# Performance work log

Hardware: AMD Instinct MI355X
Metric: run time of the kernel (lower is better)

The kernel has to match this reference:

```python
import jax, jax.numpy as jnp
import numpy as np

N = 50000      # nodes
E = 800000     # edges
IN = 128       # in_ch
OUT = 32       # out_ch
H = 4          # heads
ED = 16        # edge_dim
SLOPE = 0.2    # LeakyReLU negative slope (GATv2 default and outer activation)


def setup_inputs() -> dict:
    key = jax.random.key(0)
    ks = jax.random.split(key, 10)
    s_in = 1.0 / np.sqrt(IN)
    s_ed = 1.0 / np.sqrt(ED)
    s_out = 1.0 / np.sqrt(OUT)
    return {
        "x": jax.random.normal(ks[0], (N, IN), jnp.float32),
        "edge_index": jax.random.randint(ks[1], (2, E), 0, N, dtype=jnp.int32),
        "edges_attr": jax.random.normal(ks[2], (E, ED), jnp.float32),
        "W_l": jax.random.normal(ks[3], (IN, H * OUT), jnp.float32) * s_in,
        "b_l": jnp.zeros((H * OUT,), jnp.float32),
        "W_r": jax.random.normal(ks[4], (IN, H * OUT), jnp.float32) * s_in,
        "b_r": jnp.zeros((H * OUT,), jnp.float32),
        "W_e": jax.random.normal(ks[5], (ED, H * OUT), jnp.float32) * s_ed,
        "att": jax.random.normal(ks[6], (H, OUT), jnp.float32) * s_out,
        "bias": jnp.zeros((OUT,), jnp.float32),
    }


def reference(x, edge_index, edges_attr, W_l, b_l, W_r, b_r, W_e, att, bias):
    src, tgt = edge_index[0], edge_index[1]

    # add_self_loops with fill_value='mean': self-loop attr = scatter-mean of
    # incoming edge attrs per target node (0 for isolated nodes, as in PyG).
    deg = jax.ops.segment_sum(jnp.ones((E,), x.dtype), tgt, num_segments=N)
    attr_sum = jax.ops.segment_sum(edges_attr, tgt, num_segments=N)
    loop_attr = attr_sum / jnp.maximum(deg, 1.0)[:, None]
    node_ids = jnp.arange(N, dtype=src.dtype)
    src_f = jnp.concatenate([src, node_ids])   # [E+N]
    tgt_f = jnp.concatenate([tgt, node_ids])   # [E+N]
    attr_f = jnp.concatenate([edges_attr, loop_attr], axis=0)  # [E+N, ED]

    x_l = (x @ W_l + b_l).reshape(N, H, OUT)   # source transform
    x_r = (x @ W_r + b_r).reshape(N, H, OUT)   # target transform
    e = (attr_f @ W_e).reshape(-1, H, OUT)     # edge transform

    # GATv2 score: att . leaky_relu(x_l[j] + x_r[i] + e_ij)
    m = x_l[src_f] + x_r[tgt_f] + e                          # [E+N, H, OUT]
    scores = jnp.einsum('ehc,hc->eh', jax.nn.leaky_relu(m, SLOPE), att)

    # scatter-softmax over edges grouped by target node (every segment has a
    # self-loop, so segment_max is well-defined)
    smax = jax.ops.segment_max(scores, tgt_f, num_segments=N)
    ex = jnp.exp(scores - smax[tgt_f])
    denom = jax.ops.segment_sum(ex, tgt_f, num_segments=N)
    alpha = ex / denom[tgt_f]                                # [E+N, H]

    # weighted aggregation of source messages x_l[j]
    msg = alpha[:, :, None] * x_l[src_f]                     # [E+N, H, OUT]
    out = jax.ops.segment_sum(msg, tgt_f, num_segments=N)   # [N, H, OUT]

    out = out.mean(axis=1) + bias                            # concat=False -> head mean
    return jax.nn.leaky_relu(out, SLOPE)                     # outer LeakyReLU(0.2)
```

## Files before the change

kernel.cpp:

```cpp
#include <hip/hip_runtime.h>
#include <math.h>

#define NN 50000
#define NE 800000
#define SLOPE 0.2f
#define NB 49
#define GEMMB 782
#define EDGEB 3125


__device__ __forceinline__ void gemm_body(int bx, const float* __restrict__ x,
                                          const float* __restrict__ W,
                                          const float* __restrict__ bptr,
                                          float* __restrict__ optr,
                                          float* xs, float* wsm) {
  int tid = threadIdx.x;
  int cx = tid & 31;
  int rn = tid >> 5;
  int n0 = bx * 64;

  float acc[8][4];
#pragma unroll
  for (int i = 0; i < 8; ++i)
#pragma unroll
    for (int j = 0; j < 4; ++j) acc[i][j] = 0.f;

  for (int kb = 0; kb < 128; kb += 64) {
#pragma unroll
    for (int r = 0; r < 4; ++r) {
      int q = tid + r * 256;
      int n = q >> 4, k4 = q & 15;
      float4 v = make_float4(0.f, 0.f, 0.f, 0.f);
      int gn = n0 + n;
      if (gn < NN) v = *(const float4*)(x + (size_t)gn * 128 + kb + 4 * k4);
      *(float4*)&xs[n * 68 + 4 * k4] = v;
    }
#pragma unroll
    for (int r = 0; r < 8; ++r) {
      int q = tid + r * 256;
      int kk = q >> 5, c4 = q & 31;
      float4 wv = *(const float4*)(W + (size_t)(kb + kk) * 128 + 4 * c4);
      *(float4*)&wsm[kk * 128 + 4 * c4] = wv;
    }
    __syncthreads();
#pragma unroll 2
    for (int k4 = 0; k4 < 16; ++k4) {
      float4 wv[4];
#pragma unroll
      for (int kk = 0; kk < 4; ++kk)
        wv[kk] = *(const float4*)&wsm[(4 * k4 + kk) * 128 + 4 * cx];
#pragma unroll
      for (int i = 0; i < 8; ++i) {
        float4 xv = *(const float4*)&xs[(8 * rn + i) * 68 + 4 * k4];
        acc[i][0] = fmaf(xv.x, wv[0].x, acc[i][0]);
        acc[i][1] = fmaf(xv.x, wv[0].y, acc[i][1]);
        acc[i][2] = fmaf(xv.x, wv[0].z, acc[i][2]);
        acc[i][3] = fmaf(xv.x, wv[0].w, acc[i][3]);
        acc[i][0] = fmaf(xv.y, wv[1].x, acc[i][0]);
        acc[i][1] = fmaf(xv.y, wv[1].y, acc[i][1]);
        acc[i][2] = fmaf(xv.y, wv[1].z, acc[i][2]);
        acc[i][3] = fmaf(xv.y, wv[1].w, acc[i][3]);
        acc[i][0] = fmaf(xv.z, wv[2].x, acc[i][0]);
        acc[i][1] = fmaf(xv.z, wv[2].y, acc[i][1]);
        acc[i][2] = fmaf(xv.z, wv[2].z, acc[i][2]);
        acc[i][3] = fmaf(xv.z, wv[2].w, acc[i][3]);
        acc[i][0] = fmaf(xv.w, wv[3].x, acc[i][0]);
        acc[i][1] = fmaf(xv.w, wv[3].y, acc[i][1]);
        acc[i][2] = fmaf(xv.w, wv[3].z, acc[i][2]);
        acc[i][3] = fmaf(xv.w, wv[3].w, acc[i][3]);
      }
    }
    __syncthreads();
  }

  int cc = 4 * cx;
  float4 bv = *(const float4*)(bptr + cc);
#pragma unroll
  for (int i = 0; i < 8; ++i) {
    int gn = n0 + 8 * rn + i;
    if (gn < NN) {
      float4 o = make_float4(acc[i][0] + bv.x, acc[i][1] + bv.y,
                             acc[i][2] + bv.z, acc[i][3] + bv.w);
      *(float4*)(optr + (size_t)gn * 128 + cc) = o;
    }
  }
}


__launch_bounds__(256)
__global__ void fusedA_kernel(const float* __restrict__ x,
                              const float* __restrict__ W_l, const float* __restrict__ b_l,
                              float* __restrict__ x_l,
                              const int* __restrict__ tgt, int* __restrict__ deg,
                              int* __restrict__ rank) {
  __shared__ float xs[64 * 68];
  __shared__ float wsm[64 * 128];
  if (blockIdx.x < GEMMB) {
    gemm_body(blockIdx.x, x, W_l, b_l, x_l, xs, wsm);
  } else {
    int e = (blockIdx.x - GEMMB) * 256 + threadIdx.x;
    if (e < NE) rank[e] = atomicAdd(&deg[tgt[e]], 1);
  }
}


__launch_bounds__(256)
__global__ void fusedB_kernel(const float* __restrict__ x,
                              const float* __restrict__ W_r, const float* __restrict__ b_r,
                              float* __restrict__ x_r,
                              const int* __restrict__ src, const int* __restrict__ tgt,
                              const int* __restrict__ rank,
                              const int* __restrict__ rowptr,
                              const float4* __restrict__ eattr4,
                              int* __restrict__ csr_src,
                              float4* __restrict__ eattr_csr4) {
  __shared__ float xs[64 * 68];
  __shared__ float wsm[64 * 128];
  if (blockIdx.x < GEMMB) {
    gemm_body(blockIdx.x, x, W_r, b_r, x_r, xs, wsm);
  } else {
    int e = (blockIdx.x - GEMMB) * 256 + threadIdx.x;
    if (e < NE) {
      int t = tgt[e];
      int r = rank[e];
      float4 a0 = eattr4[(size_t)e * 4 + 0];
      float4 a1 = eattr4[(size_t)e * 4 + 1];
      float4 a2 = eattr4[(size_t)e * 4 + 2];
      float4 a3 = eattr4[(size_t)e * 4 + 3];
      int pos = rowptr[t] + r;
      csr_src[pos] = src[e];
      eattr_csr4[(size_t)pos * 4 + 0] = a0;
      eattr_csr4[(size_t)pos * 4 + 1] = a1;
      eattr_csr4[(size_t)pos * 4 + 2] = a2;
      eattr_csr4[(size_t)pos * 4 + 3] = a3;
    }
  }
}


__global__ void partial_kernel(const int* __restrict__ deg, int* __restrict__ psum) {
  int b = blockIdx.x;
  int base = b * 1024 + threadIdx.x * 4;
  int s = 0;
  if (base + 3 < NN) {
    int4 v = *(const int4*)(deg + base);
    s = v.x + v.y + v.z + v.w;
  } else {
#pragma unroll
    for (int i = 0; i < 4; ++i)
      if (base + i < NN) s += deg[base + i];
  }
  s += __shfl_xor(s, 1);
  s += __shfl_xor(s, 2);
  s += __shfl_xor(s, 4);
  s += __shfl_xor(s, 8);
  s += __shfl_xor(s, 16);
  s += __shfl_xor(s, 32);
  __shared__ int wsum[4];
  if ((threadIdx.x & 63) == 0) wsum[threadIdx.x >> 6] = s;
  __syncthreads();
  if (threadIdx.x == 0) psum[b] = wsum[0] + wsum[1] + wsum[2] + wsum[3];
}

__global__ void final_kernel(const int* __restrict__ deg, const int* __restrict__ psum,
                             int* __restrict__ rowptr) {
  __shared__ int offs_s;
  __shared__ int wtot[4];
  int b = blockIdx.x;
  int t = threadIdx.x;
  if (t < 64) {
    int lane = t;
    int mine = (lane < NB) ? psum[lane] : 0;
    int v = mine;
#pragma unroll
    for (int off = 1; off < 64; off <<= 1) {
      int u = __shfl_up(v, off);
      if (lane >= off) v += u;
    }
    if (lane == b) offs_s = v - mine;
    if (b == 0 && lane == 63) rowptr[NN] = v;
  }
  __syncthreads();

  int base = b * 1024 + t * 4;
  int d0 = 0, d1 = 0, d2 = 0, d3 = 0;
  if (base + 3 < NN) {
    int4 v = *(const int4*)(deg + base);
    d0 = v.x; d1 = v.y; d2 = v.z; d3 = v.w;
  } else {
    if (base < NN) d0 = deg[base];
    if (base + 1 < NN) d1 = deg[base + 1];
    if (base + 2 < NN) d2 = deg[base + 2];
  }
  int s = d0 + d1 + d2 + d3;
  int lane = t & 63, w = t >> 6;
  int v = s;
#pragma unroll
  for (int off = 1; off < 64; off <<= 1) {
    int u = __shfl_up(v, off);
    if (lane >= off) v += u;
  }
  if (lane == 63) wtot[w] = v;
  __syncthreads();
  int woff = 0;
#pragma unroll
  for (int i = 0; i < 4; ++i)
    if (i < w) woff += wtot[i];
  int run = offs_s + woff + (v - s);
  if (base < NN)     { rowptr[base] = run;     run += d0; }
  if (base + 1 < NN) { rowptr[base + 1] = run; run += d1; }
  if (base + 2 < NN) { rowptr[base + 2] = run; run += d2; }
  if (base + 3 < NN) { rowptr[base + 3] = run; }
}


#define EDGE_PROC(AV, XL)                                              \
  {                                                                    \
    float e0 = AV[0] * wek[0].x;                                       \
    e0 = fmaf(AV[1], wek[1].x, e0);   e0 = fmaf(AV[2], wek[2].x, e0);  \
    e0 = fmaf(AV[3], wek[3].x, e0);   e0 = fmaf(AV[4], wek[4].x, e0);  \
    e0 = fmaf(AV[5], wek[5].x, e0);   e0 = fmaf(AV[6], wek[6].x, e0);  \
    e0 = fmaf(AV[7], wek[7].x, e0);   e0 = fmaf(AV[8], wek[8].x, e0);  \
    e0 = fmaf(AV[9], wek[9].x, e0);   e0 = fmaf(AV[10], wek[10].x, e0);\
    e0 = fmaf(AV[11], wek[11].x, e0); e0 = fmaf(AV[12], wek[12].x, e0);\
    e0 = fmaf(AV[13], wek[13].x, e0); e0 = fmaf(AV[14], wek[14].x, e0);\
    e0 = fmaf(AV[15], wek[15].x, e0);                                  \
    float e1 = AV[0] * wek[0].y;                                       \
    e1 = fmaf(AV[1], wek[1].y, e1);   e1 = fmaf(AV[2], wek[2].y, e1);  \
    e1 = fmaf(AV[3], wek[3].y, e1);   e1 = fmaf(AV[4], wek[4].y, e1);  \
    e1 = fmaf(AV[5], wek[5].y, e1);   e1 = fmaf(AV[6], wek[6].y, e1);  \
    e1 = fmaf(AV[7], wek[7].y, e1);   e1 = fmaf(AV[8], wek[8].y, e1);  \
    e1 = fmaf(AV[9], wek[9].y, e1);   e1 = fmaf(AV[10], wek[10].y, e1);\
    e1 = fmaf(AV[11], wek[11].y, e1); e1 = fmaf(AV[12], wek[12].y, e1);\
    e1 = fmaf(AV[13], wek[13].y, e1); e1 = fmaf(AV[14], wek[14].y, e1);\
    e1 = fmaf(AV[15], wek[15].y, e1);                                  \
    es0 += e0; es1 += e1;                                              \
    float m0 = (XL.x + xr.x) + e0;                                     \
    float m1 = (XL.y + xr.y) + e1;                                     \
    float lm0 = fmaf(SLOPE, fminf(m0, 0.f), fmaxf(m0, 0.f));           \
    float lm1 = fmaf(SLOPE, fminf(m1, 0.f), fmaxf(m1, 0.f));           \
    float part = fmaf(attv.y, lm1, attv.x * lm0);                      \
    part += __shfl_xor(part, 1);                                       \
    part += __shfl_xor(part, 2);                                       \
    part += __shfl_xor(part, 4);                                       \
    part += __shfl_xor(part, 8);                                       \
    float p = __expf(part);                                            \
    lh += p;                                                           \
    acc0 = fmaf(p, XL.x, acc0);                                        \
    acc1 = fmaf(p, XL.y, acc1);                                        \
  }

__launch_bounds__(256)
__global__ void gat_kernel(const float* __restrict__ x_l, const float* __restrict__ x_r,
                           const int* __restrict__ rowptr, const int* __restrict__ csr_src,
                           const float* __restrict__ eattr_csr, const float* __restrict__ W_e,
                           const float* __restrict__ att, const float* __restrict__ bias,
                           float* __restrict__ out) {
  int wid = threadIdx.x >> 6;
  int lane = threadIdx.x & 63;
  int tbase = (blockIdx.x * 4 + wid) * 4;

  float2 wek[16];
#pragma unroll
  for (int k = 0; k < 16; ++k)
    wek[k] = *(const float2*)(W_e + k * 128 + 2 * lane);
  float2 attv = *(const float2*)(att + 2 * lane);
  float bv = bias[(2 * lane) & 31];
  float bv1 = bias[((2 * lane) & 31) + 1];

  for (int tt = 0; tt < 4; ++tt) {
    int t = tbase + tt;
    float2 xr = *(const float2*)(x_r + (size_t)t * 128 + 2 * lane);
    int start = __builtin_amdgcn_readfirstlane(rowptr[t]);
    int end = __builtin_amdgcn_readfirstlane(rowptr[t + 1]);

    float lh = 0.f, acc0 = 0.f, acc1 = 0.f, es0 = 0.f, es1 = 0.f;

    int j = start;
    for (; j + 4 <= end; j += 4) {
      int s0 = __builtin_amdgcn_readfirstlane(csr_src[j]);
      int s1 = __builtin_amdgcn_readfirstlane(csr_src[j + 1]);
      int s2 = __builtin_amdgcn_readfirstlane(csr_src[j + 2]);
      int s3 = __builtin_amdgcn_readfirstlane(csr_src[j + 3]);
      float2 xl0 = *(const float2*)(x_l + (size_t)s0 * 128 + 2 * lane);
      float2 xl1 = *(const float2*)(x_l + (size_t)s1 * 128 + 2 * lane);
      float2 xl2 = *(const float2*)(x_l + (size_t)s2 * 128 + 2 * lane);
      float2 xl3 = *(const float2*)(x_l + (size_t)s3 * 128 + 2 * lane);
      const float* ap0 = eattr_csr + (size_t)j * 16;
      {
        float a0[16];
#pragma unroll
        for (int k = 0; k < 16; ++k) a0[k] = ap0[k];
        EDGE_PROC(a0, xl0)
      }
      {
        float a1[16];
#pragma unroll
        for (int k = 0; k < 16; ++k) a1[k] = ap0[16 + k];
        EDGE_PROC(a1, xl1)
      }
      {
        float a2[16];
#pragma unroll
        for (int k = 0; k < 16; ++k) a2[k] = ap0[32 + k];
        EDGE_PROC(a2, xl2)
      }
      {
        float a3[16];
#pragma unroll
        for (int k = 0; k < 16; ++k) a3[k] = ap0[48 + k];
        EDGE_PROC(a3, xl3)
      }
    }
    if (j + 2 <= end) {
      int s0 = __builtin_amdgcn_readfirstlane(csr_src[j]);
      int s1 = __builtin_amdgcn_readfirstlane(csr_src[j + 1]);
      float2 xl0 = *(const float2*)(x_l + (size_t)s0 * 128 + 2 * lane);
      float2 xl1 = *(const float2*)(x_l + (size_t)s1 * 128 + 2 * lane);
      const float* ap0 = eattr_csr + (size_t)j * 16;
      {
        float a0[16];
#pragma unroll
        for (int k = 0; k < 16; ++k) a0[k] = ap0[k];
        EDGE_PROC(a0, xl0)
      }
      {
        float a1[16];
#pragma unroll
        for (int k = 0; k < 16; ++k) a1[k] = ap0[16 + k];
        EDGE_PROC(a1, xl1)
      }
      j += 2;
    }
    if (j < end) {
      int srcn = __builtin_amdgcn_readfirstlane(csr_src[j]);
      const float* ap = eattr_csr + (size_t)j * 16;
      float aC[16];
#pragma unroll
      for (int k = 0; k < 16; ++k) aC[k] = ap[k];
      float2 xlC = *(const float2*)(x_l + (size_t)srcn * 128 + 2 * lane);
      EDGE_PROC(aC, xlC)
    }

    {
      float rdeg = 1.0f / fmaxf((float)(end - start), 1.0f);
      float e0 = es0 * rdeg, e1 = es1 * rdeg;
      float2 xl = *(const float2*)(x_l + (size_t)t * 128 + 2 * lane);
      float m0 = (xl.x + xr.x) + e0;
      float m1 = (xl.y + xr.y) + e1;
      float lm0 = fmaf(SLOPE, fminf(m0, 0.f), fmaxf(m0, 0.f));
      float lm1 = fmaf(SLOPE, fminf(m1, 0.f), fmaxf(m1, 0.f));
      float part = fmaf(attv.y, lm1, attv.x * lm0);
      part += __shfl_xor(part, 1);
      part += __shfl_xor(part, 2);
      part += __shfl_xor(part, 4);
      part += __shfl_xor(part, 8);
      float p = __expf(part);
      lh += p;
      acc0 = fmaf(p, xl.x, acc0);
      acc1 = fmaf(p, xl.y, acc1);
    }

    float inv = 1.0f / lh;
    float v0 = acc0 * inv, v1 = acc1 * inv;
    v0 += __shfl_xor(v0, 16);
    v0 += __shfl_xor(v0, 32);
    v1 += __shfl_xor(v1, 16);
    v1 += __shfl_xor(v1, 32);
    if (lane < 16) {
      float o0 = fmaf(v0, 0.25f, bv);
      float o1 = fmaf(v1, 0.25f, bv1);
      o0 = fmaf(SLOPE, fminf(o0, 0.f), fmaxf(o0, 0.f));
      o1 = fmaf(SLOPE, fminf(o1, 0.f), fmaxf(o1, 0.f));
      *(float2*)(out + (size_t)t * 32 + 2 * lane) = make_float2(o0, o1);
    }
  }
}


extern "C" void kernel_launch(void* const* d_in, const int* in_sizes, int n_in,
                              void* d_out, int out_size, void* d_ws, size_t ws_size,
                              hipStream_t stream) {
  const float* x = (const float*)d_in[0];
  const int* ei = (const int*)d_in[1];
  const float* eattr = (const float*)d_in[2];
  const float* W_l = (const float*)d_in[3];
  const float* b_l = (const float*)d_in[4];
  const float* W_r = (const float*)d_in[5];
  const float* b_r = (const float*)d_in[6];
  const float* W_e = (const float*)d_in[7];
  const float* att = (const float*)d_in[8];
  const float* bias = (const float*)d_in[9];
  float* out = (float*)d_out;

  char* ws = (char*)d_ws;
  int* csr_src = (int*)ws;
  float* eattr_csr = (float*)(ws + 3200000);
  float* x_l = (float*)(ws + 54400000);
  float* x_r = (float*)(ws + 80000000);
  int* deg = (int*)(ws + 105600000);
  int* rowptr = (int*)(ws + 105800000);
  int* rank = (int*)(ws + 106000016);
  int* psum = (int*)(ws + 109200016);

  hipMemsetAsync(deg, 0, NN * sizeof(int), stream);
  fusedA_kernel<<<GEMMB + EDGEB, 256, 0, stream>>>(x, W_l, b_l, x_l, ei + NE, deg, rank);
  partial_kernel<<<NB, 256, 0, stream>>>(deg, psum);
  final_kernel<<<NB, 256, 0, stream>>>(deg, psum, rowptr);
  fusedB_kernel<<<GEMMB + EDGEB, 256, 0, stream>>>(
      x, W_r, b_r, x_r, ei, ei + NE, rank, rowptr, (const float4*)eattr,
      csr_src, (float4*)eattr_csr);
  gat_kernel<<<NN / 16, 256, 0, stream>>>(x_l, x_r, rowptr, csr_src, eattr_csr, W_e, att, bias, out);
}
```

Measured before the change: 345.9 us.

## Run node-feature GEMMs on MFMA with split-bf16 three-pass emulation

Replaces the scalar FP32 FMA tiling in the shared x@W GEMM body with bf16 MFMA 16x16x32 instructions. Each fp32 operand is split into high and low bf16 parts, and three MFMA passes (hi*hi, lo*hi, hi*lo) approximate fp32 accuracy. The LDS layout changes to bf16 tiles with K-chunks of 32. This moves the GEMM work onto matrix cores but adds conversion overhead, scalar strided loads of W, and non-vectorized output stores. It also loses a little precision compared with true fp32.

New measurement: 308.5 us. 10.8% less time.

```diff
diff --git a/kernel.cpp b/kernel.cpp
--- a/kernel.cpp
+++ b/kernel.cpp
@@ -8,80 +8,101 @@
 #define GEMMB 782
 #define EDGEB 3125
 
+typedef __attribute__((ext_vector_type(8))) short bf16x8;
+typedef __attribute__((ext_vector_type(4))) float f32x4;
+
+static __device__ __forceinline__ void split_bf16(float v, unsigned short& h,
+                                                  unsigned short& l) {
+  unsigned u = __float_as_uint(v);
+  h = (unsigned short)(u >> 16);
+  float hf = __uint_as_float(((unsigned)h) << 16);
+  float r = v - hf;
+  l = (unsigned short)(__float_as_uint(r) >> 16);
+}
+
 
 __device__ __forceinline__ void gemm_body(int bx, const float* __restrict__ x,
                                           const float* __restrict__ W,
                                           const float* __restrict__ bptr,
                                           float* __restrict__ optr,
-                                          float* xs, float* wsm) {
+                                          unsigned short* xh_s, unsigned short* xl_s,
+                                          unsigned short* wh_s, unsigned short* wl_s) {
   int tid = threadIdx.x;
-  int cx = tid & 31;
-  int rn = tid >> 5;
+  int w = tid >> 6;
+  int l = tid & 63;
   int n0 = bx * 64;
 
-  float acc[8][4];
-#pragma unroll
-  for (int i = 0; i < 8; ++i)
-#pragma unroll
-    for (int j = 0; j < 4; ++j) acc[i][j] = 0.f;
-
-  for (int kb = 0; kb < 128; kb += 64) {
+  f32x4 acc[8];
+#pragma unroll
+  for (int i = 0; i < 8; ++i) acc[i] = (f32x4){0.f, 0.f, 0.f, 0.f};
+
+  for (int kb = 0; kb < 128; kb += 32) {
+    {
+      int row = tid >> 2;
+      int kc = (tid & 3) * 8;
+      int gn = n0 + row;
+      float4 v0 = make_float4(0.f, 0.f, 0.f, 0.f);
+      float4 v1 = make_float4(0.f, 0.f, 0.f, 0.f);
+      if (gn < NN) {
+        v0 = *(const float4*)(x + (size_t)gn * 128 + kb + kc);
+        v1 = *(const float4*)(x + (size_t)gn * 128 + kb + kc + 4);
+      }
+      unsigned short h[8], lo[8];
+      split_bf16(v0.x, h[0], lo[0]); split_bf16(v0.y, h[1], lo[1]);
+      split_bf16(v0.z, h[2], lo[2]); split_bf16(v0.w, h[3], lo[3]);
+      split_bf16(v1.x, h[4], lo[4]); split_bf16(v1.y, h[5], lo[5]);
+      split_bf16(v1.z, h[6], lo[6]); split_bf16(v1.w, h[7], lo[7]);
+      bf16x8 hv, lv;
+#pragma unroll
+      for (int i = 0; i < 8; ++i) { hv[i] = (short)h[i]; lv[i] = (short)lo[i]; }
+      *(bf16x8*)&xh_s[row * 40 + kc] = hv;
+      *(bf16x8*)&xl_s[row * 40 + kc] = lv;
+    }
+    {
+      int col = tid & 127;
+      int kk0 = (tid >> 7) * 16;
+      unsigned short h[16], lo[16];
+#pragma unroll
+      for (int j = 0; j < 16; ++j)
+        split_bf16(W[(size_t)(kb + kk0 + j) * 128 + col], h[j], lo[j]);
+      bf16x8 hv0, hv1, lv0, lv1;
+#pragma unroll
+      for (int i = 0; i < 8; ++i) {
+        hv0[i] = (short)h[i]; hv1[i] = (short)h[8 + i];
+        lv0[i] = (short)lo[i]; lv1[i] = (short)lo[8 + i];
+      }
+      *(bf16x8*)&wh_s[col * 40 + kk0] = hv0;
+      *(bf16x8*)&wh_s[col * 40 + kk0 + 8] = hv1;
+      *(bf16x8*)&wl_s[col * 40 + kk0] = lv0;
+      *(bf16x8*)&wl_s[col * 40 + kk0 + 8] = lv1;
+    }
+    __syncthreads();
+
+    int r16 = 16 * w + (l & 15);
+    int ko = (l >> 4) * 8;
+    bf16x8 ah = *(bf16x8*)&xh_s[r16 * 40 + ko];
+    bf16x8 al = *(bf16x8*)&xl_s[r16 * 40 + ko];
+#pragma unroll
+    for (int ct = 0; ct < 8; ++ct) {
+      int cbase = (ct * 16 + (l & 15)) * 40 + ko;
+      bf16x8 bh = *(bf16x8*)&wh_s[cbase];
+      bf16x8 bl = *(bf16x8*)&wl_s[cbase];
+      acc[ct] = __builtin_amdgcn_mfma_f32_16x16x32_bf16(ah, bh, acc[ct], 0, 0, 0);
+      acc[ct] = __builtin_amdgcn_mfma_f32_16x16x32_bf16(al, bh, acc[ct], 0, 0, 0);
+      acc[ct] = __builtin_amdgcn_mfma_f32_16x16x32_bf16(ah, bl, acc[ct], 0, 0, 0);
+    }
+    __syncthreads();
+  }
+
+  int colb = l & 15;
+  int rq = (l >> 4) * 4;
+#pragma unroll
+  for (int ct = 0; ct < 8; ++ct) {
+    float bvv = bptr[ct * 16 + colb];
 #pragma unroll
     for (int r = 0; r < 4; ++r) {
-      int q = tid + r * 256;
-      int n = q >> 4, k4 = q & 15;
-      float4 v = make_float4(0.f, 0.f, 0.f, 0.f);
-      int gn = n0 + n;
-      if (gn < NN) v = *(const float4*)(x + (size_t)gn * 128 + kb + 4 * k4);
-      *(float4*)&xs[n * 68 + 4 * k4] = v;
-    }
-#pragma unroll
-    for (int r = 0; r < 8; ++r) {
-      int q = tid + r * 256;
-      int kk = q >> 5, c4 = q & 31;
-      float4 wv = *(const float4*)(W + (size_t)(kb + kk) * 128 + 4 * c4);
-      *(float4*)&wsm[kk * 128 + 4 * c4] = wv;
-    }
-    __syncthreads();
-#pragma unroll 2
-    for (int k4 = 0; k4 < 16; ++k4) {
-      float4 wv[4];
-#pragma unroll
-      for (int kk = 0; kk < 4; ++kk)
-        wv[kk] = *(const float4*)&wsm[(4 * k4 + kk) * 128 + 4 * cx];
-#pragma unroll
-      for (int i = 0; i < 8; ++i) {
-        float4 xv = *(const float4*)&xs[(8 * rn + i) * 68 + 4 * k4];
-        acc[i][0] = fmaf(xv.x, wv[0].x, acc[i][0]);
-        acc[i][1] = fmaf(xv.x, wv[0].y, acc[i][1]);
-        acc[i][2] = fmaf(xv.x, wv[0].z, acc[i][2]);
-        acc[i][3] = fmaf(xv.x, wv[0].w, acc[i][3]);
-        acc[i][0] = fmaf(xv.y, wv[1].x, acc[i][0]);
-        acc[i][1] = fmaf(xv.y, wv[1].y, acc[i][1]);
-        acc[i][2] = fmaf(xv.y, wv[1].z, acc[i][2]);
-        acc[i][3] = fmaf(xv.y, wv[1].w, acc[i][3]);
-        acc[i][0] = fmaf(xv.z, wv[2].x, acc[i][0]);
-        acc[i][1] = fmaf(xv.z, wv[2].y, acc[i][1]);
-        acc[i][2] = fmaf(xv.z, wv[2].z, acc[i][2]);
-        acc[i][3] = fmaf(xv.z, wv[2].w, acc[i][3]);
-        acc[i][0] = fmaf(xv.w, wv[3].x, acc[i][0]);
-        acc[i][1] = fmaf(xv.w, wv[3].y, acc[i][1]);
-        acc[i][2] = fmaf(xv.w, wv[3].z, acc[i][2]);
-        acc[i][3] = fmaf(xv.w, wv[3].w, acc[i][3]);
-      }
-    }
-    __syncthreads();
-  }
-
-  int cc = 4 * cx;
-  float4 bv = *(const float4*)(bptr + cc);
-#pragma unroll
-  for (int i = 0; i < 8; ++i) {
-    int gn = n0 + 8 * rn + i;
-    if (gn < NN) {
-      float4 o = make_float4(acc[i][0] + bv.x, acc[i][1] + bv.y,
-                             acc[i][2] + bv.z, acc[i][3] + bv.w);
-      *(float4*)(optr + (size_t)gn * 128 + cc) = o;
+      int gn = n0 + 16 * w + rq + r;
+      if (gn < NN) optr[(size_t)gn * 128 + ct * 16 + colb] = acc[ct][r] + bvv;
     }
   }
 }
@@ -93,10 +114,10 @@
                               float* __restrict__ x_l,
                               const int* __restrict__ tgt, int* __restrict__ deg,
                               int* __restrict__ rank) {
-  __shared__ float xs[64 * 68];
-  __shared__ float wsm[64 * 128];
+  __shared__ unsigned short xh_s[64 * 40], xl_s[64 * 40];
+  __shared__ unsigned short wh_s[128 * 40], wl_s[128 * 40];
   if (blockIdx.x < GEMMB) {
-    gemm_body(blockIdx.x, x, W_l, b_l, x_l, xs, wsm);
+    gemm_body(blockIdx.x, x, W_l, b_l, x_l, xh_s, xl_s, wh_s, wl_s);
   } else {
     int e = (blockIdx.x - GEMMB) * 256 + threadIdx.x;
     if (e < NE) rank[e] = atomicAdd(&deg[tgt[e]], 1);
@@ -114,10 +135,10 @@
                               const float4* __restrict__ eattr4,
                               int* __restrict__ csr_src,
                               float4* __restrict__ eattr_csr4) {
-  __shared__ float xs[64 * 68];
-  __shared__ float wsm[64 * 128];
+  __shared__ unsigned short xh_s[64 * 40], xl_s[64 * 40];
+  __shared__ unsigned short wh_s[128 * 40], wl_s[128 * 40];
   if (blockIdx.x < GEMMB) {
-    gemm_body(blockIdx.x, x, W_r, b_r, x_r, xs, wsm);
+    gemm_body(blockIdx.x, x, W_r, b_r, x_r, xh_s, xl_s, wh_s, wl_s);
   } else {
     int e = (blockIdx.x - GEMMB) * 256 + threadIdx.x;
     if (e < NE) {
```
